# Optimization experiments

Hardware: AMD Instinct MI355X
Metric: run time of the kernel (lower is better)

Reference implementation:

```python
import jax, jax.numpy as jnp
import numpy as np

BS, T, D_IN = 128, 32, 128
DH = 128          # controller hidden size == memory word width M
N_SLOTS = 512     # memory rows
EPS = 1e-8


def _split_read(o):
    # o: [bs, M+6] -> k, beta, g, s(3), gamma
    k = o[:, :DH]
    beta = jax.nn.softplus(o[:, DH])
    g = jax.nn.sigmoid(o[:, DH + 1])
    s = jax.nn.softmax(o[:, DH + 2:DH + 5], axis=-1)
    gamma = 1.0 + jax.nn.softplus(o[:, DH + 5])
    return k, beta, g, s, gamma


def _attention(k, beta, g, s, gamma, mem, w_prev):
    # content addressing: cosine similarity sharpened by beta
    dot = jnp.einsum('bnm,bm->bn', mem, k)
    denom = jnp.linalg.norm(mem, axis=-1) * jnp.linalg.norm(k, axis=-1, keepdims=True) + EPS
    w_c = jax.nn.softmax(beta[:, None] * dot / denom, axis=-1)
    # gate interpolation with previous weights
    w_g = g[:, None] * w_c + (1.0 - g[:, None]) * w_prev
    # circular shift convolution over offsets {-1, 0, +1}
    w_t = (s[:, 0:1] * jnp.roll(w_g, -1, axis=-1)
           + s[:, 1:2] * w_g
           + s[:, 2:3] * jnp.roll(w_g, 1, axis=-1))
    # sharpening
    w = w_t ** gamma[:, None]
    return w / (jnp.sum(w, axis=-1, keepdims=True) + EPS)


def setup_inputs() -> dict:
    key = jax.random.key(0)
    ks = jax.random.split(key, 8)
    sc = lambda fan_in: 1.0 / np.sqrt(fan_in)
    return {
        'x':    jax.random.normal(ks[0], (BS, T, D_IN), jnp.float32),
        'Wxh':  jax.random.normal(ks[1], (D_IN, DH), jnp.float32) * sc(D_IN),
        'Whh':  jax.random.normal(ks[2], (DH, DH), jnp.float32) * sc(DH),
        'Wrh':  jax.random.normal(ks[3], (DH, DH), jnp.float32) * sc(DH),
        'bh':   jnp.zeros((DH,), jnp.float32),
        'Wout': jax.random.normal(ks[4], (DH + DH, D_IN), jnp.float32) * sc(2 * DH),
        'bout': jnp.zeros((D_IN,), jnp.float32),
        'Wr':   jax.random.normal(ks[5], (DH, DH + 6), jnp.float32) * sc(DH),
        'br':   jnp.zeros((DH + 6,), jnp.float32),
        'Ww':   jax.random.normal(ks[6], (DH, 3 * DH + 6), jnp.float32) * sc(DH),
        'bw':   jnp.zeros((3 * DH + 6,), jnp.float32),
    }


def reference(x, Wxh, Whh, Wrh, bh, Wout, bout, Wr, br, Ww, bw):
    bs = x.shape[0]
    h0 = jnp.zeros((bs, DH), x.dtype)
    r0 = jnp.zeros((bs, DH), x.dtype)
    w0 = jnp.full((bs, N_SLOTS), 1.0 / N_SLOTS, x.dtype)
    mem0 = jnp.full((bs, N_SLOTS, DH), 1e-6, x.dtype)

    def step(carry, x_t):
        h, r, w_prev, mem = carry
        # controller state
        h = jnp.tanh(x_t @ Wxh + h @ Whh + r @ Wrh + bh)
        # head parameter projections
        o_r = h @ Wr + br
        o_w = h @ Ww + bw
        k_r, b_r, g_r, s_r, y_r = _split_read(o_r)
        k_w, b_w_, g_w, s_w, y_w = _split_read(o_w[:, :DH + 6])
        e = jax.nn.sigmoid(o_w[:, DH + 6:2 * DH + 6])   # erase [bs, M]
        a = jnp.tanh(o_w[:, 2 * DH + 6:3 * DH + 6])     # add   [bs, M]
        # addressing (w_previous updated sequentially, read then write)
        w_r = _attention(k_r, b_r, g_r, s_r, y_r, mem, w_prev)
        w_w = _attention(k_w, b_w_, g_w, s_w, y_w, mem, w_r)
        # read
        r = jnp.einsum('bn,bnm->bm', w_r, mem)
        # erase / add write
        mem = mem * (1.0 - w_w[:, :, None] * e[:, None, :]) + w_w[:, :, None] * a[:, None, :]
        # output
        y = jnp.concatenate([h, r], axis=-1) @ Wout + bout
        return (h, r, w_w, mem), y

    _, ys = jax.lax.scan(step, (h0, r0, w0, mem0), jnp.swapaxes(x, 0, 1))
    return jnp.swapaxes(ys, 0, 1)  # [bs, ft, d_output]
```

## Files before the change

### kernel.cpp

```cpp
#include <hip/hip_runtime.h>
#include <hip/hip_bf16.h>
#include <math.h>

#define NT 1024
#define BSZ 128
#define TSTEPS 32
#define DIN 128
#define DHH 128
#define NSLOT 512
#define EPSF 1e-8f

static constexpr int F_FLOATS = 7160;
static constexpr size_t LDS_BYTES = 131072 + F_FLOATS * sizeof(float);

__device__ __forceinline__ float bf_lo(unsigned u) {
  union { unsigned u; float f; } c; c.u = u << 16; return c.f;
}
__device__ __forceinline__ float bf_hi(unsigned u) {
  union { unsigned u; float f; } c; c.u = u & 0xffff0000u; return c.f;
}
__device__ __forceinline__ unsigned short f2us(float f) {
  union { unsigned short s; __hip_bfloat16 h; } c; c.h = __float2bfloat16(f); return c.s;
}
__device__ __forceinline__ unsigned pkbf(float a, float b) {
  union { __hip_bfloat162 h2; unsigned u; } c;
  c.h2 = __float22bfloat162_rn(make_float2(a, b));
  return c.u;
}
__device__ __forceinline__ float sigmoid_(float x) { return 1.0f / (1.0f + __expf(-x)); }
__device__ __forceinline__ float softplus_(float x) {
  return fmaxf(x, 0.0f) + log1pf(__expf(-fabsf(x)));
}
__device__ __forceinline__ float tanh_(float x) {
  float e = __expf(-2.0f * fabsf(x));
  float t = (1.0f - e) / (1.0f + e);
  return copysignf(t, x);
}
__device__ __forceinline__ float waveSum(float v) {
#pragma unroll
  for (int m = 32; m >= 1; m >>= 1) v += __shfl_xor(v, m);
  return v;
}

__global__ __launch_bounds__(NT, 4)
void ntm_kernel(const float* __restrict__ x,
                const float* __restrict__ Wxh,
                const float* __restrict__ Whh,
                const float* __restrict__ Wrh,
                const float* __restrict__ bh,
                const float* __restrict__ Wout,
                const float* __restrict__ bout,
                const float* __restrict__ Wr,
                const float* __restrict__ br,
                const float* __restrict__ Ww,
                const float* __restrict__ bw,
                float* __restrict__ out)
{
  extern __shared__ char smem[];
  uint4* memv = (uint4*)smem;
  float* F = (float*)(smem + 131072);

  const int b = blockIdx.x;
  const int tid = threadIdx.x;
  const int g = tid >> 4, l = tid & 15;
  const int lane = tid & 63, wid = tid >> 6;

  float* U      = F + 0;
  float* yP     = F + 2560;
  float* sWprev = F + 4608;
  float* sWr    = F + 5120;
  float* sP1    = F + 5632;
  float* sOr    = F + 6144;
  float* sOw    = F + 6288;
  float* sH     = F + 6680;
  float* sR     = F + 6808;
  float* sXt    = F + 6936;
  float* sP     = F + 7064;
  uint4* krP    = (uint4*)(sP1 + 0);
  uint4* kwP    = (uint4*)(sP1 + 64);
  float* eR     = U + 0;
  float* eW     = U + 512;

  {
    const unsigned short mb = f2us(1e-6f);
    const unsigned w32 = ((unsigned)mb << 16) | mb;
    const uint4 fv = make_uint4(w32, w32, w32, w32);
    for (int i = tid; i < NSLOT * DHH / 8; i += NT) memv[i] = fv;
  }
  for (int i = tid; i < NSLOT; i += NT) sWprev[i] = 1.0f / NSLOT;
  if (tid < DHH) { sH[tid] = 0.0f; sR[tid] = 0.0f; }
  if (tid < DIN) sXt[tid] = x[(size_t)b * TSTEPS * DIN + tid];
  __syncthreads();

  for (int t = 0; t < TSTEPS; ++t) {
    {
      const int q = tid & 63, s = tid >> 6;
      const int j2 = q * 2, i0 = s * 24;
      float2 acc = make_float2(0.f, 0.f);
#pragma unroll 8
      for (int w = 0; w < 24; ++w) {
        const int i = i0 + w;
        float v; const float* Wp;
        if (i < 128)      { v = sXt[i];       Wp = Wxh + i * DHH; }
        else if (i < 256) { v = sH[i - 128];  Wp = Whh + (i - 128) * DHH; }
        else              { v = sR[i - 256];  Wp = Wrh + (i - 256) * DHH; }
        const float2 wv = *(const float2*)(Wp + j2);
        acc.x = fmaf(v, wv.x, acc.x);
        acc.y = fmaf(v, wv.y, acc.y);
      }
      *(float2*)(U + s * 128 + j2) = acc;
      __syncthreads();
    }
    if (tid < DHH) {
      float a2 = bh[tid];
#pragma unroll
      for (int q2 = 0; q2 < 16; ++q2) a2 += U[q2 * 128 + tid];
      sH[tid] = tanh_(a2);
    }
    __syncthreads();

    {
      {
        const int s = tid;
        const int q = (s >= 786) ? 3 : (s >= 524) ? 2 : (s >= 262) ? 1 : 0;
        const int P = s - 262 * q;
        const int i0 = 32 * q;
        const float2* p;
        int strideF2;
        if (P < 67) { p = (const float2*)(Wr + i0 * 134 + 2 * P); strideF2 = 67; }
        else        { p = (const float2*)(Ww + i0 * 390 + 2 * (P - 67)); strideF2 = 195; }
        float2 acc = make_float2(0.f, 0.f);
#pragma unroll 8
        for (int w = 0; w < 32; ++w) {
          const float v = sH[i0 + w];
          const float2 wv = *p;
          acc.x = fmaf(v, wv.x, acc.x);
          acc.y = fmaf(v, wv.y, acc.y);
          p += strideF2;
        }
        *(float2*)(U + s * 2) = acc;
      }
      if (lane < 3) {
        const int hs = wid * 3 + lane;
        const int e = hs >> 1, hh = hs & 1;
        const int cp = 171 + e;
        const int i0 = 96 + 16 * hh;
        const float2* p = (const float2*)(Ww + i0 * 390 + 2 * cp);
        float2 acc = make_float2(0.f, 0.f);
#pragma unroll 8
        for (int w = 0; w < 16; ++w) {
          const float v = sH[i0 + w];
          const float2 wv = *p;
          acc.x = fmaf(v, wv.x, acc.x);
          acc.y = fmaf(v, wv.y, acc.y);
          p += 195;
        }
        U[2096 + hs * 2]     = acc.x;
        U[2096 + hs * 2 + 1] = acc.y;
      }
      if (tid == 1023) {
        sP[0] = 0.f; sP[1] = 0.f; sP[2] = 0.f; sP[3] = 0.f; sP[4] = 0.f; sP[5] = 0.f;
      }
      __syncthreads();
    }

    {
      if (tid < 134) {
        float v = 0.f;
#pragma unroll
        for (int q = 0; q < 4; ++q) v += U[tid + 524 * q];
        v += br[tid];
        sOr[tid] = v;
        if (tid < 128) {
          float s2 = waveSum(v * v);
          if (lane == 0) atomicAdd(&sP[0], s2);
        }
      } else if (tid == 134) {
        float sc[6];
#pragma unroll
        for (int j = 0; j < 6; ++j) {
          float v = 0.f;
#pragma unroll
          for (int q = 0; q < 4; ++q) v += U[(128 + j) + 524 * q];
          sc[j] = v + br[128 + j];
        }
        sP[80] = softplus_(sc[0]);
        sP[81] = sigmoid_(sc[1]);
        float mx = fmaxf(sc[2], fmaxf(sc[3], sc[4]));
        float e0 = __expf(sc[2] - mx), e1 = __expf(sc[3] - mx), e2 = __expf(sc[4] - mx);
        float es = e0 + e1 + e2;
        sP[82] = e0 / es; sP[83] = e1 / es; sP[84] = e2 / es;
        sP[85] = 1.0f + softplus_(sc[5]);
      } else if (tid == 135) {
        float sc[6];
#pragma unroll
        for (int j = 0; j < 6; ++j) {
          float v = 0.f;
#pragma unroll
          for (int q = 0; q < 4; ++q) v += U[(262 + j) + 524 * q];
          sc[j] = v + bw[128 + j];
        }
        sP[86] = softplus_(sc[0]);
        sP[87] = sigmoid_(sc[1]);
        float mx = fmaxf(sc[2], fmaxf(sc[3], sc[4]));
        float e0 = __expf(sc[2] - mx), e1 = __expf(sc[3] - mx), e2 = __expf(sc[4] - mx);
        float es = e0 + e1 + e2;
        sP[88] = e0 / es; sP[89] = e1 / es; sP[90] = e2 / es;
        sP[91] = 1.0f + softplus_(sc[5]);
      } else if (tid >= 256 && tid < 512) {
        const int cc = tid + 12;
        float v = U[cc] + U[cc + 524] + U[cc + 1048];
        if (cc < 476) {
          v += U[cc + 1572];
        } else {
          const int cw = cc - 134;
          const int e = (cw >> 1) - 171;
          const int base = 2096 + 4 * e + (cw & 1);
          v += U[base] + U[base + 2];
        }
        v += bw[tid - 122];
        sOw[tid - 120] = (tid < 384) ? sigmoid_(v) : tanh_(v);
      } else if (tid >= 512 && tid < 640) {
        const int cw = tid - 512;
        float v = 0.f;
#pragma unroll
        for (int q = 0; q < 4; ++q) v += U[(134 + cw) + 524 * q];
        v += bw[cw];
        sOw[cw] = v;
        float s2 = waveSum(v * v);
        if (lane == 0) atomicAdd(&sP[1], s2);
      } else if (tid >= 640 && tid < 768) {
        sR[tid - 640] = 0.f;
      } else if (tid >= 768 && tid < 800) {
        const int t2 = tid - 768;
        const int c = t2 & 15;
        union { uint4 v; unsigned short h[8]; } pk;
#pragma unroll
        for (int j = 0; j < 8; ++j) {
          const int col = c * 8 + j;
          float v = 0.f;
#pragma unroll
          for (int q = 0; q < 4; ++q)
            v += U[((t2 < 16) ? col : (134 + col)) + 524 * q];
          v += (t2 < 16) ? br[col] : bw[col];
          pk.h[j] = f2us(v);
        }
        if (t2 < 16) krP[c] = pk.v; else kwP[c] = pk.v;
      } else if (tid >= 896) {
        if (t > 0) {
          const int c = tid - 896;
          float y = bout[c];
#pragma unroll
          for (int q = 0; q < 16; ++q) y += yP[q * 128 + c];
          out[((size_t)b * TSTEPS + (t - 1)) * DIN + c] = y;
        }
      }
      __syncthreads();
    }

    {
      const float kn_r = sqrtf(sP[0]);
      const float kn_w = sqrtf(sP[1]);
      const float beta_r = sP[80], beta_w = sP[86];
      const int n = tid >> 1, hf = tid & 1;
      const int sw = (n >> 2) & 3;
      float dr = 0.f, dw = 0.f, ss = 0.f;
#pragma unroll
      for (int c = 0; c < 8; ++c) {
        const int cl = hf * 8 + c;
        const uint4 mv = memv[n * 16 + (cl ^ sw)];
        const uint4 kr = krP[cl];
        const uint4 kw = kwP[cl];
        const unsigned mw_[4] = { mv.x, mv.y, mv.z, mv.w };
        const unsigned krw[4] = { kr.x, kr.y, kr.z, kr.w };
        const unsigned kww[4] = { kw.x, kw.y, kw.z, kw.w };
#pragma unroll
        for (int j = 0; j < 4; ++j) {
          const float m0 = bf_lo(mw_[j]), m1 = bf_hi(mw_[j]);
          dr = fmaf(m0, bf_lo(krw[j]), dr); dr = fmaf(m1, bf_hi(krw[j]), dr);
          dw = fmaf(m0, bf_lo(kww[j]), dw); dw = fmaf(m1, bf_hi(kww[j]), dw);
          ss = fmaf(m0, m0, ss);            ss = fmaf(m1, m1, ss);
        }
      }
      dr += __shfl_xor(dr, 1);
      dw += __shfl_xor(dw, 1);
      ss += __shfl_xor(ss, 1);
      const float nr = sqrtf(ss);
      const float er = __expf(beta_r * dr / (nr * kn_r + EPSF));
      const float ew = __expf(beta_w * dw / (nr * kn_w + EPSF));
      if (hf == 0) { eR[n] = er; eW[n] = ew; }
      float s1 = waveSum(er) * 0.5f;
      float s2 = waveSum(ew) * 0.5f;
      if (lane == 0) { atomicAdd(&sP[2], s1); atomicAdd(&sP[3], s2); }
      __syncthreads();
    }

    {
      if (tid < NSLOT) {
        const float invE = 1.0f / sP[2];
        const float gr = sP[81], omg = 1.0f - sP[81];
        const int im = (tid - 1) & 511, ip = (tid + 1) & 511;
        const float wgm = gr * (eR[im] * invE) + omg * sWprev[im];
        const float wg0 = gr * (eR[tid] * invE) + omg * sWprev[tid];
        const float wgp = gr * (eR[ip] * invE) + omg * sWprev[ip];
        const float wt = sP[82] * wgp + sP[83] * wg0 + sP[84] * wgm;
        float p1 = (wt > 0.0f) ? __expf(sP[85] * __logf(wt)) : 0.0f;
        float P = waveSum(p1);
        sP1[tid] = p1;
        if (lane == 0) atomicAdd(&sP[4], P);
      } else {
        const int p = tid - 512;
        const int j4 = (p & 31) * 4, sl = p >> 5;
        float4 acc = make_float4(0.f, 0.f, 0.f, 0.f);
#pragma unroll
        for (int w = 0; w < 8; ++w) {
          const float v = sH[8 * sl + w];
          const float4 wv = *(const float4*)(Wout + (8 * sl + w) * DIN + j4);
          acc.x = fmaf(v, wv.x, acc.x); acc.y = fmaf(v, wv.y, acc.y);
          acc.z = fmaf(v, wv.z, acc.z); acc.w = fmaf(v, wv.w, acc.w);
        }
        *(float4*)(yP + sl * 128 + j4) = acc;
      }
      __syncthreads();
    }
    {
      if (tid < NSLOT) {
        const float pinv1 = 1.0f / (sP[4] + EPSF);
        const float invE = 1.0f / sP[3];
        const float gw = sP[87], omg = 1.0f - sP[87];
        const int im = (tid - 1) & 511, ip = (tid + 1) & 511;
        const float wgm = gw * (eW[im] * invE) + omg * (sP1[im] * pinv1);
        const float wg0 = gw * (eW[tid] * invE) + omg * (sP1[tid] * pinv1);
        const float wgp = gw * (eW[ip] * invE) + omg * (sP1[ip] * pinv1);
        sWr[tid] = sP1[tid] * pinv1;
        const float wt = sP[88] * wgp + sP[89] * wg0 + sP[90] * wgm;
        float p2 = (wt > 0.0f) ? __expf(sP[91] * __logf(wt)) : 0.0f;
        float P = waveSum(p2);
        U[tid] = p2;
        if (lane == 0) atomicAdd(&sP[5], P);
      } else if (tid < 512 + DIN && t + 1 < TSTEPS) {
        const int i = tid - 512;
        sXt[i] = x[((size_t)b * TSTEPS + (t + 1)) * DIN + i];
      }
      __syncthreads();
    }

    {
      const float pinv2 = 1.0f / (sP[5] + EPSF);
      if (tid < NSLOT) sWprev[tid] = U[tid] * pinv2;

      const int cl = l ^ ((g >> 2) & 3);
      float4 e4a = *(const float4*)(sOw + 136 + cl * 8);
      float4 e4b = *(const float4*)(sOw + 140 + cl * 8);
      float4 a4a = *(const float4*)(sOw + 264 + cl * 8);
      float4 a4b = *(const float4*)(sOw + 268 + cl * 8);
      const float e8[8] = { e4a.x, e4a.y, e4a.z, e4a.w, e4b.x, e4b.y, e4b.z, e4b.w };
      const float a8[8] = { a4a.x, a4a.y, a4a.z, a4a.w, a4b.x, a4b.y, a4b.z, a4b.w };
      float r8[8] = { 0, 0, 0, 0, 0, 0, 0, 0 };
#pragma unroll 2
      for (int it = 0; it < 8; ++it) {
        const int n = g + 64 * it;
        const float wrn = sWr[n];
        const float wwn = U[n] * pinv2;
        uint4 pk = memv[n * 16 + l];
        const unsigned wds[4] = { pk.x, pk.y, pk.z, pk.w };
        float m[8];
#pragma unroll
        for (int j = 0; j < 4; ++j) { m[2 * j] = bf_lo(wds[j]); m[2 * j + 1] = bf_hi(wds[j]); }
#pragma unroll
        for (int j = 0; j < 8; ++j) {
          r8[j] = fmaf(wrn, m[j], r8[j]);
          const float d = fmaf(-e8[j], m[j], a8[j]);
          m[j] = fmaf(wwn, d, m[j]);
        }
        pk.x = pkbf(m[0], m[1]);
        pk.y = pkbf(m[2], m[3]);
        pk.z = pkbf(m[4], m[5]);
        pk.w = pkbf(m[6], m[7]);
        memv[n * 16 + l] = pk;
      }
#pragma unroll
      for (int j = 0; j < 8; ++j) {
        r8[j] += __shfl_xor(r8[j], 16);
        r8[j] += __shfl_xor(r8[j], 32);
      }
      if (lane < 16) {
#pragma unroll
        for (int j = 0; j < 8; ++j) atomicAdd(&sR[cl * 8 + j], r8[j]);
      }
      __syncthreads();
    }

    {
      if (tid < 512) {
        const int j4 = (tid & 31) * 4, sl = tid >> 5;
        float4 acc = *(const float4*)(yP + sl * 128 + j4);
#pragma unroll
        for (int w = 0; w < 8; ++w) {
          const float v = sR[8 * sl + w];
          const float4 wv = *(const float4*)(Wout + (128 + 8 * sl + w) * DIN + j4);
          acc.x = fmaf(v, wv.x, acc.x); acc.y = fmaf(v, wv.y, acc.y);
          acc.z = fmaf(v, wv.z, acc.z); acc.w = fmaf(v, wv.w, acc.w);
        }
        *(float4*)(yP + sl * 128 + j4) = acc;
      }
      __syncthreads();
    }
  }

  if (tid < DIN) {
    float y = bout[tid];
#pragma unroll
    for (int q = 0; q < 16; ++q) y += yP[q * 128 + tid];
    out[((size_t)b * TSTEPS + (TSTEPS - 1)) * DIN + tid] = y;
  }
}

extern "C" void kernel_launch(void* const* d_in, const int* in_sizes, int n_in,
                              void* d_out, int out_size, void* d_ws, size_t ws_size,
                              hipStream_t stream) {
  (void)in_sizes; (void)n_in; (void)out_size; (void)d_ws; (void)ws_size;
  hipFuncSetAttribute(reinterpret_cast<const void*>(ntm_kernel),
                      hipFuncAttributeMaxDynamicSharedMemorySize, (int)LDS_BYTES);
  ntm_kernel<<<dim3(BSZ), dim3(NT), LDS_BYTES, stream>>>(
      (const float*)d_in[0], (const float*)d_in[1], (const float*)d_in[2],
      (const float*)d_in[3], (const float*)d_in[4], (const float*)d_in[5],
      (const float*)d_in[6], (const float*)d_in[7], (const float*)d_in[8],
      (const float*)d_in[9], (const float*)d_in[10],
      (float*)d_out);
}
```

Before: 858.4 us.

## Prefetch weight tiles into registers a phase early and use LDS-only barriers

Each phase's global weight loads (controller, head projections, output projection) are now issued into registers during the preceding phase, so their latency overlaps the earlier barrier and compute instead of sitting on the critical path. __syncthreads is replaced by a barrier that only waits on LDS counters, so outstanding global prefetches do not stall it. sXt, sH and sR are reordered to be contiguous so the controller matvec reads vector inputs as float4. The cost is much higher register pressure (w1, w3, wtop, wbot arrays) at 1024 threads, which risks spills or lower occupancy.

```diff
diff --git a/kernel.cpp b/kernel.cpp
--- a/kernel.cpp
+++ b/kernel.cpp
@@ -40,6 +40,11 @@
 #pragma unroll
   for (int m = 32; m >= 1; m >>= 1) v += __shfl_xor(v, m);
   return v;
+}
+
+__device__ __forceinline__ void bar_lds() {
+  asm volatile("s_waitcnt lgkmcnt(0)" ::: "memory");
+  __builtin_amdgcn_s_barrier();
 }
 
 __global__ __launch_bounds__(NT, 4)
@@ -72,14 +77,32 @@
   float* sP1    = F + 5632;
   float* sOr    = F + 6144;
   float* sOw    = F + 6288;
-  float* sH     = F + 6680;
-  float* sR     = F + 6808;
-  float* sXt    = F + 6936;
+  float* sXt    = F + 6680;
+  float* sH     = F + 6808;
+  float* sR     = F + 6936;
   float* sP     = F + 7064;
+  float* V      = sXt;
   uint4* krP    = (uint4*)(sP1 + 0);
   uint4* kwP    = (uint4*)(sP1 + 64);
   float* eR     = U + 0;
   float* eW     = U + 512;
+
+  const int s1  = tid >> 6;
+  const int j2s = (tid & 63) * 2;
+  const int i0s = s1 * 24;
+  const int q3  = (tid >= 786) ? 3 : (tid >= 524) ? 2 : (tid >= 262) ? 1 : 0;
+  const int P3  = tid - 262 * q3;
+  const int i03 = 32 * q3;
+  const float2* p3base;
+  int stride3;
+  if (P3 < 67) { p3base = (const float2*)(Wr + i03 * 134 + 2 * P3); stride3 = 67; }
+  else         { p3base = (const float2*)(Ww + i03 * 390 + 2 * (P3 - 67)); stride3 = 195; }
+  const int hs   = wid * 3 + lane;
+  const int i0h  = 96 + 16 * (hs & 1);
+  const int cph2 = 2 * (171 + (hs >> 1));
+  const int pT  = tid - 512;
+  const int j4T = (pT & 31) * 4, slT = pT >> 5;
+  const int j4B = (tid & 31) * 4, slB = tid >> 5;
 
   {
     const unsigned short mb = f2us(1e-6f);
@@ -92,24 +115,48 @@
   if (tid < DIN) sXt[tid] = x[(size_t)b * TSTEPS * DIN + tid];
   __syncthreads();
 
+  float2 w1[24];
+#define LOAD_W1()                                                          \
+  do {                                                                     \
+    _Pragma("unroll")                                                      \
+    for (int w = 0; w < 24; ++w) {                                         \
+      const int i = i0s + w;                                               \
+      const float* Wp = (i < 128) ? (Wxh + i * DHH)                        \
+                      : (i < 256) ? (Whh + (i - 128) * DHH)                \
+                                  : (Wrh + (i - 256) * DHH);               \
+      w1[w] = *(const float2*)(Wp + j2s);                                  \
+    }                                                                      \
+  } while (0)
+
+  LOAD_W1();
+
   for (int t = 0; t < TSTEPS; ++t) {
-    {
-      const int q = tid & 63, s = tid >> 6;
-      const int j2 = q * 2, i0 = s * 24;
+    float2 w3[32];
+    float2 w3h[16];
+    float4 wtop[8];
+    float4 wbot[8];
+
+    {
       float2 acc = make_float2(0.f, 0.f);
-#pragma unroll 8
-      for (int w = 0; w < 24; ++w) {
-        const int i = i0 + w;
-        float v; const float* Wp;
-        if (i < 128)      { v = sXt[i];       Wp = Wxh + i * DHH; }
-        else if (i < 256) { v = sH[i - 128];  Wp = Whh + (i - 128) * DHH; }
-        else              { v = sR[i - 256];  Wp = Wrh + (i - 256) * DHH; }
-        const float2 wv = *(const float2*)(Wp + j2);
-        acc.x = fmaf(v, wv.x, acc.x);
-        acc.y = fmaf(v, wv.y, acc.y);
-      }
-      *(float2*)(U + s * 128 + j2) = acc;
-      __syncthreads();
+#pragma unroll
+      for (int k = 0; k < 6; ++k) {
+        const float4 vv = *(const float4*)(V + i0s + 4 * k);
+        const float vk[4] = { vv.x, vv.y, vv.z, vv.w };
+#pragma unroll
+        for (int u = 0; u < 4; ++u) {
+          acc.x = fmaf(vk[u], w1[4 * k + u].x, acc.x);
+          acc.y = fmaf(vk[u], w1[4 * k + u].y, acc.y);
+        }
+      }
+      *(float2*)(U + s1 * 128 + j2s) = acc;
+      if (lane < 3) {
+#pragma unroll
+        for (int w = 0; w < 16; ++w)
+          w3h[w] = *(const float2*)(Ww + (i0h + w) * 390 + cph2);
+      }
+#pragma unroll
+      for (int w = 0; w < 32; ++w) w3[w] = p3base[w * stride3];
+      bar_lds();
     }
     if (tid < DHH) {
       float a2 = bh[tid];
@@ -117,54 +164,48 @@
       for (int q2 = 0; q2 < 16; ++q2) a2 += U[q2 * 128 + tid];
       sH[tid] = tanh_(a2);
     }
-    __syncthreads();
-
-    {
-      {
-        const int s = tid;
-        const int q = (s >= 786) ? 3 : (s >= 524) ? 2 : (s >= 262) ? 1 : 0;
-        const int P = s - 262 * q;
-        const int i0 = 32 * q;
-        const float2* p;
-        int strideF2;
-        if (P < 67) { p = (const float2*)(Wr + i0 * 134 + 2 * P); strideF2 = 67; }
-        else        { p = (const float2*)(Ww + i0 * 390 + 2 * (P - 67)); strideF2 = 195; }
-        float2 acc = make_float2(0.f, 0.f);
-#pragma unroll 8
-        for (int w = 0; w < 32; ++w) {
-          const float v = sH[i0 + w];
-          const float2 wv = *p;
-          acc.x = fmaf(v, wv.x, acc.x);
-          acc.y = fmaf(v, wv.y, acc.y);
-          p += strideF2;
-        }
-        *(float2*)(U + s * 2) = acc;
-      }
+    bar_lds();
+
+    {
+      float2 acc = make_float2(0.f, 0.f);
+#pragma unroll
+      for (int k = 0; k < 8; ++k) {
+        const float4 hv = *(const float4*)(sH + i03 + 4 * k);
+        const float hk[4] = { hv.x, hv.y, hv.z, hv.w };
+#pragma unroll
+        for (int u = 0; u < 4; ++u) {
+          acc.x = fmaf(hk[u], w3[4 * k + u].x, acc.x);
+          acc.y = fmaf(hk[u], w3[4 * k + u].y, acc.y);
+        }
+      }
+      *(float2*)(U + tid * 2) = acc;
       if (lane < 3) {
-        const int hs = wid * 3 + lane;
-        const int e = hs >> 1, hh = hs & 1;
-        const int cp = 171 + e;
-        const int i0 = 96 + 16 * hh;
-        const float2* p = (const float2*)(Ww + i0 * 390 + 2 * cp);
-        float2 acc = make_float2(0.f, 0.f);
-#pragma unroll 8
-        for (int w = 0; w < 16; ++w) {
-          const float v = sH[i0 + w];
-          const float2 wv = *p;
-          acc.x = fmaf(v, wv.x, acc.x);
-          acc.y = fmaf(v, wv.y, acc.y);
-          p += 195;
-        }
-        U[2096 + hs * 2]     = acc.x;
-        U[2096 + hs * 2 + 1] = acc.y;
+        float2 acch = make_float2(0.f, 0.f);
+#pragma unroll
+        for (int k = 0; k < 4; ++k) {
+          const float4 hv = *(const float4*)(sH + i0h + 4 * k);
+          const float hk[4] = { hv.x, hv.y, hv.z, hv.w };
+#pragma unroll
+          for (int u = 0; u < 4; ++u) {
+            acch.x = fmaf(hk[u], w3h[4 * k + u].x, acch.x);
+            acch.y = fmaf(hk[u], w3h[4 * k + u].y, acch.y);
+          }
+        }
+        U[2096 + hs * 2]     = acch.x;
+        U[2096 + hs * 2 + 1] = acch.y;
       }
       if (tid == 1023) {
         sP[0] = 0.f; sP[1] = 0.f; sP[2] = 0.f; sP[3] = 0.f; sP[4] = 0.f; sP[5] = 0.f;
       }
-      __syncthreads();
-    }
-
-    {
+      bar_lds();
+    }
+
+    {
+      if (tid >= 512) {
+#pragma unroll
+        for (int w = 0; w < 8; ++w)
+          wtop[w] = *(const float4*)(Wout + (8 * slT + w) * DIN + j4T);
+      }
       if (tid < 134) {
         float v = 0.f;
 #pragma unroll
@@ -255,7 +296,7 @@
           out[((size_t)b * TSTEPS + (t - 1)) * DIN + c] = y;
         }
       }
-      __syncthreads();
+      bar_lds();
     }
 
     {
@@ -289,10 +330,10 @@
       const float er = __expf(beta_r * dr / (nr * kn_r + EPSF));
       const float ew = __expf(beta_w * dw / (nr * kn_w + EPSF));
       if (hf == 0) { eR[n] = er; eW[n] = ew; }
-      float s1 = waveSum(er) * 0.5f;
-      float s2 = waveSum(ew) * 0.5f;
-      if (lane == 0) { atomicAdd(&sP[2], s1); atomicAdd(&sP[3], s2); }
-      __syncthreads();
+      float s1_ = waveSum(er) * 0.5f;
+      float s2_ = waveSum(ew) * 0.5f;
+      if (lane == 0) { atomicAdd(&sP[2], s1_); atomicAdd(&sP[3], s2_); }
+      bar_lds();
     }
 
     {
@@ -309,22 +350,24 @@
         sP1[tid] = p1;
         if (lane == 0) atomicAdd(&sP[4], P);
       } else {
-        const int p = tid - 512;
-        const int j4 = (p & 31) * 4, sl = p >> 5;
         float4 acc = make_float4(0.f, 0.f, 0.f, 0.f);
+        const float4 ha = *(const float4*)(sH + 8 * slT);
+        const float4 hb = *(const float4*)(sH + 8 * slT + 4);
+        const float hv[8] = { ha.x, ha.y, ha.z, ha.w, hb.x, hb.y, hb.z, hb.w };
 #pragma unroll
         for (int w = 0; w < 8; ++w) {
-          const float v = sH[8 * sl + w];
-          const float4 wv = *(const float4*)(Wout + (8 * sl + w) * DIN + j4);
-          acc.x = fmaf(v, wv.x, acc.x); acc.y = fmaf(v, wv.y, acc.y);
-          acc.z = fmaf(v, wv.z, acc.z); acc.w = fmaf(v, wv.w, acc.w);
-        }
-        *(float4*)(yP + sl * 128 + j4) = acc;
-      }
-      __syncthreads();
+          acc.x = fmaf(hv[w], wtop[w].x, acc.x); acc.y = fmaf(hv[w], wtop[w].y, acc.y);
+          acc.z = fmaf(hv[w], wtop[w].z, acc.z); acc.w = fmaf(hv[w], wtop[w].w, acc.w);
+        }
+        *(float4*)(yP + slT * 128 + j4T) = acc;
+      }
+      bar_lds();
     }
     {
       if (tid < NSLOT) {
+#pragma unroll
+        for (int w = 0; w < 8; ++w)
+          wbot[w] = *(const float4*)(Wout + (128 + 8 * slB + w) * DIN + j4B);
         const float pinv1 = 1.0f / (sP[4] + EPSF);
         const float invE = 1.0f / sP[3];
         const float gw = sP[87], omg = 1.0f - sP[87];
@@ -342,7 +385,7 @@
         const int i = tid - 512;
         sXt[i] = x[((size_t)b * TSTEPS + (t + 1)) * DIN + i];
       }
-      __syncthreads();
+      bar_lds();
     }
 
     {
@@ -388,23 +431,24 @@
 #pragma unroll
         for (int j = 0; j < 8; ++j) atomicAdd(&sR[cl * 8 + j], r8[j]);
       }
-      __syncthreads();
+      LOAD_W1();
+      bar_lds();
     }
 
     {
       if (tid < 512) {
-        const int j4 = (tid & 31) * 4, sl = tid >> 5;
-        float4 acc = *(const float4*)(yP + sl * 128 + j4);
+        float4 acc = *(const float4*)(yP + slB * 128 + j4B);
+        const float4 ra = *(const float4*)(sR + 8 * slB);
+        const float4 rb = *(const float4*)(sR + 8 * slB + 4);
+        const float rv[8] = { ra.x, ra.y, ra.z, ra.w, rb.x, rb.y, rb.z, rb.w };
 #pragma unroll
         for (int w = 0; w < 8; ++w) {
-          const float v = sR[8 * sl + w];
-          const float4 wv = *(const float4*)(Wout + (128 + 8 * sl + w) * DIN + j4);
-          acc.x = fmaf(v, wv.x, acc.x); acc.y = fmaf(v, wv.y, acc.y);
-          acc.z = fmaf(v, wv.z, acc.z); acc.w = fmaf(v, wv.w, acc.w);
-        }
-        *(float4*)(yP + sl * 128 + j4) = acc;
-      }
-      __syncthreads();
+          acc.x = fmaf(rv[w], wbot[w].x, acc.x); acc.y = fmaf(rv[w], wbot[w].y, acc.y);
+          acc.z = fmaf(rv[w], wbot[w].z, acc.z); acc.w = fmaf(rv[w], wbot[w].w, acc.w);
+        }
+        *(float4*)(yP + slB * 128 + j4B) = acc;
+      }
+      bar_lds();
     }
   }
 
```

After: 2.062 ms. 140% more time.
